# Kernel optimization log

Measured on AMD Instinct MI355X. Metric: run time of the kernel, lower is better.

## Reference

```python
import jax, jax.numpy as jnp
import numpy as np


def setup_inputs() -> dict:
    key = jax.random.key(0)
    k1, k2 = jax.random.split(key)
    x = jax.random.normal(k1, (4096, 1024), dtype=jnp.float32)  # [B, D] queries
    y = jax.random.normal(k2, (8192, 1024), dtype=jnp.float32)  # [N, D] database
    return {"x": x, "y": y}


def reference(x, y):
    # -sum((x[:, None, :] - y[None, :, :])**2, -1)  computed via the
    x_sq = jnp.sum(x * x, axis=-1)              # [B]
    y_sq = jnp.sum(y * y, axis=-1)              # [N]
    xy = jnp.einsum('bd,nd->bn', x, y)          # [B, N]
    return -(x_sq[:, None] - 2.0 * xy + y_sq[None, :])  # [B, N]
```

## Files before the change

kernel.cpp:

```cpp
#include <hip/hip_runtime.h>
#include <hip/hip_bf16.h>


typedef __attribute__((ext_vector_type(4))) int i32x4;

#define BM 256
#define BN 256
#define KD 1024
#define NT 8

__device__ __forceinline__ void gld16(const void* g, void* l) {
    __builtin_amdgcn_global_load_lds(
        (const __attribute__((address_space(1))) unsigned int*)g,
        (__attribute__((address_space(3))) unsigned int*)l,
        16, 0, 0);
}

#define BAR() asm volatile("s_barrier" ::: "memory")

__global__ __launch_bounds__(256) void prep_q(
    const float* __restrict__ x, const float* __restrict__ y,
    signed char* __restrict__ xq, signed char* __restrict__ yq,
    float* __restrict__ sx, float* __restrict__ sy,
    float* __restrict__ xsq, float* __restrict__ ysq, int M, int N)
{
    int row = blockIdx.x;
    const float* src;
    signed char* dst;
    float* nrm;
    float* scl;
    float sfac;
    if (row < M) {
        src = x + (size_t)row * KD; dst = xq + (size_t)row * KD;
        nrm = xsq + row; scl = sx + row; sfac = 2.0f;
    } else {
        int r = row - M;
        src = y + (size_t)r * KD; dst = yq + (size_t)r * KD;
        nrm = ysq + r; scl = sy + r; sfac = 1.0f;
    }
    int t = threadIdx.x;
    float4 v = ((const float4*)src)[t];
    float ss = v.x * v.x + v.y * v.y + v.z * v.z + v.w * v.w;
    float am = fmaxf(fmaxf(fabsf(v.x), fabsf(v.y)),
                     fmaxf(fabsf(v.z), fabsf(v.w)));
    #pragma unroll
    for (int off = 32; off > 0; off >>= 1) {
        ss += __shfl_down(ss, off, 64);
        am = fmaxf(am, __shfl_down(am, off, 64));
    }
    __shared__ float rs[4], rm[4];
    if ((t & 63) == 0) { rs[t >> 6] = ss; rm[t >> 6] = am; }
    __syncthreads();
    float tots = rs[0] + rs[1] + rs[2] + rs[3];
    float totm = fmaxf(fmaxf(rm[0], rm[1]), fmaxf(rm[2], rm[3]));
    float inv = totm > 0.0f ? 127.0f / totm : 0.0f;

    int q0 = (int)rintf(v.x * inv), q1 = (int)rintf(v.y * inv);
    int q2 = (int)rintf(v.z * inv), q3 = (int)rintf(v.w * inv);
    q0 = max(-127, min(127, q0)); q1 = max(-127, min(127, q1));
    q2 = max(-127, min(127, q2)); q3 = max(-127, min(127, q3));
    int packed = (q0 & 255) | ((q1 & 255) << 8) |
                 ((q2 & 255) << 16) | ((q3 & 255) << 24);
    ((int*)dst)[t] = packed;
    if (t == 0) { *nrm = tots; *scl = sfac * totm / 127.0f; }
}

__global__ __launch_bounds__(512, 2) void gemm_i8(
    const signed char* __restrict__ xq, const signed char* __restrict__ yq,
    const float* __restrict__ sx, const float* __restrict__ sy,
    const float* __restrict__ xsq, const float* __restrict__ ysq,
    float* __restrict__ out, int M, int N)
{
    __shared__ __align__(16) char lds[131072];

    const int ntm = M / BM;
    const int ntn = N / BN;
    const int bid = blockIdx.x;
    int tm, tn;
    if (ntm == 16 && ntn == 32) {
        int xcd = bid & 7, k = bid >> 3;
        tm = (xcd >> 2) * 8 + (k >> 3);
        tn = (xcd & 3) * 8 + (k & 7);
    } else {
        tm = bid / ntn;
        tn = bid % ntn;
    }

    const int tid  = threadIdx.x;
    const int wid  = tid >> 6;
    const int lane = tid & 63;
    const int wm   = wid >> 2;
    const int wn   = wid & 3;
    const int l15  = lane & 15;
    const int hi   = lane >> 4;
    const int s8   = lane & 7;

    const int r8  = lane >> 3;
    const int cbs = s8 ^ (r8 & 7);
    const signed char* aBase = xq + (size_t)(tm * BM + wid * 16 + r8) * KD + cbs * 16;
    const signed char* bBase = yq + (size_t)(tn * BN + wid * 16 + r8) * KD + cbs * 16;
    const int dstBase = wid * 2048 + lane * 16;

    #define STAGE_A(kt, h) do {                                               \
        const signed char* g_ = aBase + (size_t)(h) * 128 * KD + (size_t)(kt) * 128; \
        char* d_ = &lds[((kt) & 1) * 32768 + (h) * 16384 + dstBase];          \
        gld16(g_, d_); gld16(g_ + 8 * KD, d_ + 1024);                         \
    } while (0)
    #define STAGE_B(kt, h) do {                                               \
        const signed char* g_ = bBase + (size_t)(h) * 128 * KD + (size_t)(kt) * 128; \
        char* d_ = &lds[65536 + ((kt) & 1) * 32768 + (h) * 16384 + dstBase];  \
        gld16(g_, d_); gld16(g_ + 8 * KD, d_ + 1024);                         \
    } while (0)

    int aro[4], bro[2], xk[2];
    #pragma unroll
    for (int i = 0; i < 4; ++i) aro[i] = (wm * 64 + i * 16 + l15) * 128;
    #pragma unroll
    for (int j = 0; j < 2; ++j) bro[j] = (wn * 32 + j * 16 + l15) * 128;
    xk[0] = ((0 + hi) ^ s8) * 16;
    xk[1] = ((4 + hi) ^ s8) * 16;

    i32x4 acc[2][4][2][2] = {};
    i32x4 fA0[8], fB0[4];
    i32x4 fA1[8], fB1[4];

    #define READS(FA, FB, AB, BB, KS) do {                                   \
        _Pragma("unroll") for (int h = 0; h < 2; ++h)                        \
        _Pragma("unroll") for (int i = 0; i < 4; ++i)                        \
            FA[h * 4 + i] = *(const i32x4*)&lds[(AB) + h * 16384 + aro[i] + xk[KS]]; \
        _Pragma("unroll") for (int h = 0; h < 2; ++h)                        \
        _Pragma("unroll") for (int j = 0; j < 2; ++j)                        \
            FB[h * 2 + j] = *(const i32x4*)&lds[(BB) + h * 16384 + bro[j] + xk[KS]]; \
    } while (0)

    #define MFMA_SET(FA, FB) do {                                            \
        __builtin_amdgcn_s_setprio(1);                                       \
        _Pragma("unroll") for (int mq = 0; mq < 2; ++mq)                     \
        _Pragma("unroll") for (int i = 0; i < 4; ++i)                        \
        _Pragma("unroll") for (int nq = 0; nq < 2; ++nq)                     \
        _Pragma("unroll") for (int j = 0; j < 2; ++j)                        \
            acc[mq][i][nq][j] = __builtin_amdgcn_mfma_i32_16x16x64_i8(       \
                FA[mq * 4 + i], FB[nq * 2 + j], acc[mq][i][nq][j], 0, 0, 0); \
        __builtin_amdgcn_s_setprio(0);                                       \
    } while (0)

    STAGE_A(0, 0); STAGE_A(0, 1); STAGE_B(0, 0); STAGE_B(0, 1);
    asm volatile("s_waitcnt vmcnt(0)" ::: "memory");
    BAR();
    READS(fA0, fB0, 0, 65536, 0);

    #pragma unroll
    for (int k = 0; k < NT; ++k) {
        const int ab  = (k & 1) * 32768;
        const int bb  = 65536 + ab;
        const int abn = ((k + 1) & 1) * 32768;
        const int bbn = 65536 + abn;

        if (k + 1 < NT) {
            STAGE_A(k + 1, 0); STAGE_A(k + 1, 1);
            STAGE_B(k + 1, 0); STAGE_B(k + 1, 1);
        }
        READS(fA1, fB1, ab, bb, 1);
        MFMA_SET(fA0, fB0);

        if (k + 1 < NT) {
            asm volatile("s_waitcnt vmcnt(0)" ::: "memory");
            BAR();
            READS(fA0, fB0, abn, bbn, 0);
        }
        MFMA_SET(fA1, fB1);
    }

    #pragma unroll
    for (int mq = 0; mq < 2; ++mq)
        #pragma unroll
        for (int i = 0; i < 4; ++i) {
            int r0 = tm * BM + mq * 128 + wm * 64 + i * 16 + hi * 4;
            #pragma unroll
            for (int nq = 0; nq < 2; ++nq)
                #pragma unroll
                for (int j = 0; j < 2; ++j) {
                    int c = tn * BN + nq * 128 + wn * 32 + j * 16 + l15;
                    float syv = sy[c];
                    float ysv = ysq[c];
                    #pragma unroll
                    for (int r = 0; r < 4; ++r) {
                        int row = r0 + r;
                        out[(size_t)row * N + c] =
                            sx[row] * syv * (float)acc[mq][i][nq][j][r]
                            - xsq[row] - ysv;
                    }
                }
        }
}

__global__ __launch_bounds__(256) void fallback_l2(
    const float* __restrict__ x, const float* __restrict__ y,
    float* __restrict__ out, int M, int N, int K)
{
    int tx = threadIdx.x & 15, ty = threadIdx.x >> 4;
    int row = blockIdx.y * 16 + ty;
    int col = blockIdx.x * 16 + tx;
    __shared__ float xs[16][17], ys[16][17];
    float s = 0.f;
    for (int k0 = 0; k0 < K; k0 += 16) {
        xs[ty][tx] = x[(size_t)row * K + k0 + tx];
        ys[ty][tx] = y[(size_t)(blockIdx.x * 16 + ty) * K + k0 + tx];
        __syncthreads();
        #pragma unroll
        for (int kk = 0; kk < 16; ++kk) {
            float d = xs[ty][kk] - ys[tx][kk];
            s += d * d;
        }
        __syncthreads();
    }
    out[(size_t)row * N + col] = -s;
}

extern "C" void kernel_launch(void* const* d_in, const int* in_sizes, int n_in,
                              void* d_out, int out_size, void* d_ws, size_t ws_size,
                              hipStream_t stream) {
    const float* x = (const float*)d_in[0];
    const float* y = (const float*)d_in[1];
    float* out = (float*)d_out;
    const int M = in_sizes[0] / KD;
    const int N = in_sizes[1] / KD;

    size_t need = (size_t)(M + N) * KD
                + (size_t)(M + N) * 2 * sizeof(float) + 256;
    if (ws_size >= need && M == 4096 && N == 8192) {
        char* w = (char*)d_ws;
        signed char* xq = (signed char*)w;
        signed char* yq = xq + (size_t)M * KD;
        float* sx  = (float*)(yq + (size_t)N * KD);
        float* sy  = sx + M;
        float* xsq = sy + N;
        float* ysq = xsq + M;

        prep_q<<<M + N, 256, 0, stream>>>(x, y, xq, yq, sx, sy, xsq, ysq, M, N);
        int grid = (M / BM) * (N / BN);
        gemm_i8<<<grid, 512, 0, stream>>>(xq, yq, sx, sy, xsq, ysq, out, M, N);
    } else {
        dim3 g(N / 16, M / 16);
        fallback_l2<<<g, 256, 0, stream>>>(x, y, out, M, N, KD);
    }
}
```

Baseline: 64.14 us.

## Switch int8 GEMM to 32x32x32 MFMA tiles and deepen prefetch by one stage

Replaces the 16x16x64 int8 MFMA accumulation with 32x32x32 int8 MFMAs, remapping each wave's LDS fragment offsets and the epilogue row/column layout to match. The larger instruction tile is meant to raise operand reuse per LDS read and cut instruction count. The global-to-LDS staging now issues two tiles up front and starts the k+2 load after the barrier, overlapping loads across more compute. The new vmcnt accounting and double-buffer reuse timing must stay correct, or loads could race with reads of the buffer being overwritten.

After: 70.20 us. 1.09x slower.

```diff
diff --git a/kernel.cpp b/kernel.cpp
--- a/kernel.cpp
+++ b/kernel.cpp
@@ -2,7 +2,8 @@
 #include <hip/hip_bf16.h>
 
 
-typedef __attribute__((ext_vector_type(4))) int i32x4;
+typedef __attribute__((ext_vector_type(4)))  int i32x4;
+typedef __attribute__((ext_vector_type(16))) int i32x16;
 
 #define BM 256
 #define BN 256
@@ -91,8 +92,8 @@
     const int lane = tid & 63;
     const int wm   = wid >> 2;
     const int wn   = wid & 3;
-    const int l15  = lane & 15;
-    const int hi   = lane >> 4;
+    const int l31  = lane & 31;
+    const int hi5  = lane >> 5;
     const int s8   = lane & 7;
 
     const int r8  = lane >> 3;
@@ -111,87 +112,83 @@
         char* d_ = &lds[65536 + ((kt) & 1) * 32768 + (h) * 16384 + dstBase];  \
         gld16(g_, d_); gld16(g_ + 8 * KD, d_ + 1024);                         \
     } while (0)
-
-    int aro[4], bro[2], xk[2];
-    #pragma unroll
-    for (int i = 0; i < 4; ++i) aro[i] = (wm * 64 + i * 16 + l15) * 128;
-    #pragma unroll
-    for (int j = 0; j < 2; ++j) bro[j] = (wn * 32 + j * 16 + l15) * 128;
-    xk[0] = ((0 + hi) ^ s8) * 16;
-    xk[1] = ((4 + hi) ^ s8) * 16;
-
-    i32x4 acc[2][4][2][2] = {};
+    #define STAGE(kt) do { STAGE_A(kt, 0); STAGE_A(kt, 1);                    \
+                           STAGE_B(kt, 0); STAGE_B(kt, 1); } while (0)
+
+    int aoff[4], boff[2], xk[4];
+    #pragma unroll
+    for (int mi = 0; mi < 4; ++mi)
+        aoff[mi] = wm * 16384 + (mi * 32 + l31) * 128;
+    #pragma unroll
+    for (int nj = 0; nj < 2; ++nj)
+        boff[nj] = (wn >> 1) * 16384 + ((wn & 1) * 64 + nj * 32 + l31) * 128;
+    #pragma unroll
+    for (int s = 0; s < 4; ++s)
+        xk[s] = ((s * 2 + hi5) ^ (l31 & 7)) * 16;
+
+    i32x16 acc[4][2] = {};
     i32x4 fA0[8], fB0[4];
     i32x4 fA1[8], fB1[4];
 
-    #define READS(FA, FB, AB, BB, KS) do {                                   \
-        _Pragma("unroll") for (int h = 0; h < 2; ++h)                        \
-        _Pragma("unroll") for (int i = 0; i < 4; ++i)                        \
-            FA[h * 4 + i] = *(const i32x4*)&lds[(AB) + h * 16384 + aro[i] + xk[KS]]; \
-        _Pragma("unroll") for (int h = 0; h < 2; ++h)                        \
-        _Pragma("unroll") for (int j = 0; j < 2; ++j)                        \
-            FB[h * 2 + j] = *(const i32x4*)&lds[(BB) + h * 16384 + bro[j] + xk[KS]]; \
+    #define READS(FA, FB, AB, KS) do {                                       \
+        _Pragma("unroll") for (int sl = 0; sl < 2; ++sl) {                   \
+            const int s_ = (KS) * 2 + sl;                                    \
+            _Pragma("unroll") for (int mi = 0; mi < 4; ++mi)                 \
+                FA[sl * 4 + mi] = *(const i32x4*)&lds[(AB) + aoff[mi] + xk[s_]]; \
+            _Pragma("unroll") for (int nj = 0; nj < 2; ++nj)                 \
+                FB[sl * 2 + nj] = *(const i32x4*)&lds[65536 + (AB) + boff[nj] + xk[s_]]; \
+        }                                                                    \
     } while (0)
 
     #define MFMA_SET(FA, FB) do {                                            \
         __builtin_amdgcn_s_setprio(1);                                       \
-        _Pragma("unroll") for (int mq = 0; mq < 2; ++mq)                     \
-        _Pragma("unroll") for (int i = 0; i < 4; ++i)                        \
-        _Pragma("unroll") for (int nq = 0; nq < 2; ++nq)                     \
-        _Pragma("unroll") for (int j = 0; j < 2; ++j)                        \
-            acc[mq][i][nq][j] = __builtin_amdgcn_mfma_i32_16x16x64_i8(       \
-                FA[mq * 4 + i], FB[nq * 2 + j], acc[mq][i][nq][j], 0, 0, 0); \
+        _Pragma("unroll") for (int sl = 0; sl < 2; ++sl)                     \
+        _Pragma("unroll") for (int mi = 0; mi < 4; ++mi)                     \
+        _Pragma("unroll") for (int nj = 0; nj < 2; ++nj)                     \
+            acc[mi][nj] = __builtin_amdgcn_mfma_i32_32x32x32_i8(             \
+                FA[sl * 4 + mi], FB[sl * 2 + nj], acc[mi][nj], 0, 0, 0);     \
         __builtin_amdgcn_s_setprio(0);                                       \
     } while (0)
 
-    STAGE_A(0, 0); STAGE_A(0, 1); STAGE_B(0, 0); STAGE_B(0, 1);
-    asm volatile("s_waitcnt vmcnt(0)" ::: "memory");
+    STAGE(0);
+    STAGE(1);
+    asm volatile("s_waitcnt vmcnt(8)" ::: "memory");
     BAR();
-    READS(fA0, fB0, 0, 65536, 0);
+    READS(fA0, fB0, 0, 0);
 
     #pragma unroll
     for (int k = 0; k < NT; ++k) {
         const int ab  = (k & 1) * 32768;
-        const int bb  = 65536 + ab;
         const int abn = ((k + 1) & 1) * 32768;
-        const int bbn = 65536 + abn;
-
-        if (k + 1 < NT) {
-            STAGE_A(k + 1, 0); STAGE_A(k + 1, 1);
-            STAGE_B(k + 1, 0); STAGE_B(k + 1, 1);
-        }
-        READS(fA1, fB1, ab, bb, 1);
+
+        READS(fA1, fB1, ab, 1);
         MFMA_SET(fA0, fB0);
 
         if (k + 1 < NT) {
             asm volatile("s_waitcnt vmcnt(0)" ::: "memory");
             BAR();
-            READS(fA0, fB0, abn, bbn, 0);
+            READS(fA0, fB0, abn, 0);
+            if (k + 2 < NT) STAGE(k + 2);
         }
         MFMA_SET(fA1, fB1);
     }
 
     #pragma unroll
-    for (int mq = 0; mq < 2; ++mq)
+    for (int mi = 0; mi < 4; ++mi) {
+        int rb = tm * BM + wm * 128 + mi * 32 + hi5 * 4;
         #pragma unroll
-        for (int i = 0; i < 4; ++i) {
-            int r0 = tm * BM + mq * 128 + wm * 64 + i * 16 + hi * 4;
+        for (int nj = 0; nj < 2; ++nj) {
+            int c = tn * BN + wn * 64 + nj * 32 + l31;
+            float syv = sy[c];
+            float ysv = ysq[c];
             #pragma unroll
-            for (int nq = 0; nq < 2; ++nq)
-                #pragma unroll
-                for (int j = 0; j < 2; ++j) {
-                    int c = tn * BN + nq * 128 + wn * 32 + j * 16 + l15;
-                    float syv = sy[c];
-                    float ysv = ysq[c];
-                    #pragma unroll
-                    for (int r = 0; r < 4; ++r) {
-                        int row = r0 + r;
-                        out[(size_t)row * N + c] =
-                            sx[row] * syv * (float)acc[mq][i][nq][j][r]
-                            - xsq[row] - ysv;
-                    }
-                }
+            for (int r = 0; r < 16; ++r) {
+                int row = rb + (r & 3) + 8 * (r >> 2);
+                out[(size_t)row * N + c] =
+                    sx[row] * syv * (float)acc[mi][nj][r] - xsq[row] - ysv;
+            }
         }
+    }
 }
 
 __global__ __launch_bounds__(256) void fallback_l2(
```
